# Performance work log

Hardware: AMD Instinct MI355X
Metric: run time of the kernel (lower is better)

The kernel has to match this reference:

```python
import jax, jax.numpy as jnp
import numpy as np

L1 = 0.05
L2 = 0.05
L3 = 0.05
L4 = 0.05
D_MIN = 1.0
EPS = 1e-12


def _pairwise_dist(x, y):
    sq = (jnp.sum(x * x, axis=-1)[:, None]
          + jnp.sum(y * y, axis=-1)[None, :]
          - 2.0 * (x @ y.T))
    return jnp.sqrt(jnp.clip(sq, EPS))


def setup_inputs() -> dict:
    key = jax.random.key(0)
    k1, k2, k3, k4, k5, k6 = jax.random.split(key, 6)
    B, C, D, d, P = 32768, 100, 1024, 512, 128
    return {
        "predictions": jax.random.normal(k1, (B, C), dtype=jnp.float32),
        "reconstructions": jax.random.normal(k2, (B, D), dtype=jnp.float32),
        "data": jax.random.normal(k3, (B, D), dtype=jnp.float32),
        "embeddings": jax.random.normal(k4, (B, d), dtype=jnp.float32),
        "prototypes": jax.random.normal(k5, (P, d), dtype=jnp.float32),
        "labels": jax.random.randint(k6, (B,), 0, C, dtype=jnp.int64),
    }


def reference(predictions, reconstructions, data, embeddings, prototypes, labels):
    B = predictions.shape[0]
    P = prototypes.shape[0]

    # Cross-entropy (mean reduction, class-index targets)
    logp = jax.nn.log_softmax(predictions, axis=-1)
    classification_loss = -jnp.mean(logp[jnp.arange(B), labels])

    # MSE reconstruction loss (mean reduction)
    reconstruction_loss = jnp.mean((reconstructions - data) ** 2)

    # Prototype diversity penalty: sum_{j<k} max(0, d_min - ||p_j - p_k||)^2
    proto_dist = _pairwise_dist(prototypes, prototypes)  # [P, P]
    hinge = jnp.maximum(0.0, D_MIN - proto_dist) ** 2
    upper = jnp.triu(jnp.ones((P, P), dtype=bool), k=1)
    diversity_penalty = jnp.sum(jnp.where(upper, hinge, 0.0))

    # Embedding-to-prototype distances [B, P], shared by similarity/coverage penalties
    dist = _pairwise_dist(embeddings, prototypes)
    similarity_penalty = jnp.sum(jnp.min(dist, axis=0)) / P
    coverage_penalty = jnp.sum(jnp.min(dist, axis=1)) / B

    total_loss = (classification_loss
                  + L1 * reconstruction_loss
                  + L2 * diversity_penalty
                  + L3 * similarity_penalty
                  + L4 * coverage_penalty)
    return total_loss
```

## Files before the change

### kernel.cpp

```cpp
#include <hip/hip_runtime.h>
#include <hip/hip_bf16.h>


constexpr float FEPS = 1e-12f;
constexpr float DMIN = 1.0f;

#define NB_DIST 512
#define NB_MSE  1024
#define NB_CE   256
#define NB_DIV  128

typedef unsigned short ushort_t;
typedef __attribute__((ext_vector_type(8))) short bf16x8;
typedef __attribute__((ext_vector_type(8))) unsigned short u16x8;
typedef __attribute__((ext_vector_type(4))) unsigned short u16x4;
typedef __attribute__((ext_vector_type(16))) float f32x16;
typedef __attribute__((ext_vector_type(4))) float f32x4;

typedef __attribute__((address_space(1))) const void gvoid_t;
typedef __attribute__((address_space(3))) void lvoid_t;

__device__ __forceinline__ unsigned short f2b(float f) {
    unsigned u = __float_as_uint(f);
    u += 0x7FFFu + ((u >> 16) & 1u);
    return (unsigned short)(u >> 16);
}

union SmemU {
    struct {
        char     As[8192];
        char     Bs[2 * 16384];
        float    rown[64];
        float    pn[128];
        unsigned rowmin[64];
        unsigned colmin[128];
    } dist;
    struct { float pp[512]; float spp; float sred[4]; } div;
    struct { float sred[4]; } red;
};

__global__ __launch_bounds__(128) void conv_kernel(const float* __restrict__ proto,
                                                   ushort_t* __restrict__ pB,
                                                   float* __restrict__ pnorm,
                                                   float* __restrict__ ws,
                                                   unsigned* __restrict__ proto_min) {
    int p = blockIdx.x, q = threadIdx.x;
    if (q == 0) proto_min[p] = 0x7F7F7F7Fu;
    if (p == 0 && q < 4) ws[q] = 0.f;
    float4 v = ((const float4*)(proto + (size_t)p * 512))[q];
    u16x4 o = { f2b(v.x), f2b(v.y), f2b(v.z), f2b(v.w) };
    *(u16x4*)(pB + (size_t)p * 512 + q * 4) = o;
    float s = v.x * v.x + v.y * v.y + v.z * v.z + v.w * v.w;
    #pragma unroll
    for (int off = 32; off; off >>= 1) s += __shfl_xor(s, off);
    __shared__ float sr[2];
    if ((q & 63) == 0) sr[q >> 6] = s;
    __syncthreads();
    if (q == 0) pnorm[p] = sr[0] + sr[1];
}

__device__ __forceinline__ void dist_body_fast(SmemU& sm, int bid,
                                               const float* __restrict__ emb,
                                               const ushort_t* __restrict__ pB,
                                               const float* __restrict__ pnormG,
                                               unsigned* __restrict__ proto_min,
                                               float* __restrict__ cov_out) {
    char*     AsB     = sm.dist.As;
    char*     BsB     = sm.dist.Bs;
    float*    rownL   = sm.dist.rown;
    float*    pnL     = sm.dist.pn;
    unsigned* rowminL = sm.dist.rowmin;
    unsigned* colminL = sm.dist.colmin;

    const int t  = threadIdx.x;
    const int m0 = bid * 64;

    if (t < 64)  { rownL[t] = 0.f; rowminL[t] = 0x7F7F7F7Fu; }
    if (t < 128) { colminL[t] = 0x7F7F7F7Fu; pnL[t] = pnormG[t]; }

    int aidx[4], rowi[4], swzi[4];
    const float4* embF4 = (const float4*)emb;
    #pragma unroll
    for (int i = 0; i < 4; ++i) {
        int flat = i * 256 + t;
        int row = flat >> 4, colq = flat & 15;
        rowi[i] = row;
        aidx[i] = (m0 + row) * 128 + colq;
        swzi[i] = row * 128 + ((((colq >> 1) ^ (row & 7)) << 4) | ((colq & 1) << 3));
    }

    const ushort_t* bsrcp[4];
    char* bdstW[4];
    #pragma unroll
    for (int i = 0; i < 4; ++i) {
        int f = i * 256 + t;
        int pr = f >> 3, gb = f & 7;
        bsrcp[i] = pB + pr * 512 + ((gb ^ (pr & 7)) << 3);
        bdstW[i] = BsB + (size_t)(i * 256 + (t & ~63)) * 16;
    }

    const int lane = t & 63, wv = t >> 6;
    const int wr = wv >> 1, wc = wv & 1;
    const int lo = lane & 31, hi = lane >> 5;
    const int arow = wr * 32 + lo;
    const int arz  = arow & 7;
    const int p0 = wc * 64 + lo, p1 = p0 + 32;
    const int pz = p0 & 7;
    const char* Ar  = AsB + arow * 128;
    const char* Br0 = BsB + p0 * 128;
    const char* Br1 = BsB + p1 * 128;

    __builtin_amdgcn_global_load_lds((gvoid_t*)(bsrcp[0]), (lvoid_t*)bdstW[0], 16, 0, 0);
    __builtin_amdgcn_global_load_lds((gvoid_t*)(bsrcp[1]), (lvoid_t*)bdstW[1], 16, 0, 0);
    __builtin_amdgcn_global_load_lds((gvoid_t*)(bsrcp[2]), (lvoid_t*)bdstW[2], 16, 0, 0);
    __builtin_amdgcn_global_load_lds((gvoid_t*)(bsrcp[3]), (lvoid_t*)bdstW[3], 16, 0, 0);
    float4 aE0 = embF4[aidx[0]], aE1 = embF4[aidx[1]],
           aE2 = embF4[aidx[2]], aE3 = embF4[aidx[3]];
    float4 aO0, aO1, aO2, aO3;
    float rn0 = 0.f, rn1 = 0.f, rn2 = 0.f, rn3 = 0.f;
    f32x16 acc0 = {}, acc1 = {};
    asm volatile("s_waitcnt lgkmcnt(0)" ::: "memory");
    __builtin_amdgcn_s_barrier();
    __builtin_amdgcn_sched_barrier(0);

#define DIST_CHUNK(c, WAITN, W0, W1, W2, W3, L0, L1, L2, L3)                   \
    {                                                                          \
        if ((c) < 7) {                                                         \
            const int kc1 = ((c) + 1) * 64;                                    \
            const int bo1 = (((c) + 1) & 1) * 16384;                           \
            __builtin_amdgcn_global_load_lds((gvoid_t*)(bsrcp[0] + kc1),       \
                (lvoid_t*)(bdstW[0] + bo1), 16, 0, 0);                         \
            __builtin_amdgcn_global_load_lds((gvoid_t*)(bsrcp[1] + kc1),       \
                (lvoid_t*)(bdstW[1] + bo1), 16, 0, 0);                         \
            __builtin_amdgcn_global_load_lds((gvoid_t*)(bsrcp[2] + kc1),       \
                (lvoid_t*)(bdstW[2] + bo1), 16, 0, 0);                         \
            __builtin_amdgcn_global_load_lds((gvoid_t*)(bsrcp[3] + kc1),       \
                (lvoid_t*)(bdstW[3] + bo1), 16, 0, 0);                         \
        }                                                                      \
        __builtin_amdgcn_sched_barrier(0);                                     \
        {                                                                      \
            const int kn = ((c) < 7 ? (c) + 1 : 7) * 16;                       \
            L0 = embF4[aidx[0] + kn]; L1 = embF4[aidx[1] + kn];                \
            L2 = embF4[aidx[2] + kn]; L3 = embF4[aidx[3] + kn];                \
        }                                                                      \
        __builtin_amdgcn_sched_barrier(0);                                     \
        rn0 = fmaf(W0.x, W0.x, rn0); rn0 = fmaf(W0.y, W0.y, rn0);              \
        rn0 = fmaf(W0.z, W0.z, rn0); rn0 = fmaf(W0.w, W0.w, rn0);              \
        rn1 = fmaf(W1.x, W1.x, rn1); rn1 = fmaf(W1.y, W1.y, rn1);              \
        rn1 = fmaf(W1.z, W1.z, rn1); rn1 = fmaf(W1.w, W1.w, rn1);              \
        rn2 = fmaf(W2.x, W2.x, rn2); rn2 = fmaf(W2.y, W2.y, rn2);              \
        rn2 = fmaf(W2.z, W2.z, rn2); rn2 = fmaf(W2.w, W2.w, rn2);              \
        rn3 = fmaf(W3.x, W3.x, rn3); rn3 = fmaf(W3.y, W3.y, rn3);              \
        rn3 = fmaf(W3.z, W3.z, rn3); rn3 = fmaf(W3.w, W3.w, rn3);              \
        { u16x4 u = { f2b(W0.x), f2b(W0.y), f2b(W0.z), f2b(W0.w) };            \
          *(u16x4*)(AsB + swzi[0]) = u; }                                      \
        { u16x4 u = { f2b(W1.x), f2b(W1.y), f2b(W1.z), f2b(W1.w) };            \
          *(u16x4*)(AsB + swzi[1]) = u; }                                      \
        { u16x4 u = { f2b(W2.x), f2b(W2.y), f2b(W2.z), f2b(W2.w) };            \
          *(u16x4*)(AsB + swzi[2]) = u; }                                      \
        { u16x4 u = { f2b(W3.x), f2b(W3.y), f2b(W3.z), f2b(W3.w) };            \
          *(u16x4*)(AsB + swzi[3]) = u; }                                      \
        asm volatile("s_waitcnt vmcnt(" #WAITN ")" ::: "memory");              \
        asm volatile("s_waitcnt lgkmcnt(0)" ::: "memory");                     \
        __builtin_amdgcn_s_barrier();                                          \
        __builtin_amdgcn_sched_barrier(0);                                     \
        {                                                                      \
            const int bo = ((c) & 1) * 16384;                                  \
            _Pragma("unroll")                                                  \
            for (int s = 0; s < 4; ++s) {                                      \
                const int g = (s * 2 + hi);                                    \
                bf16x8 af = *(const bf16x8*)(Ar  + ((g ^ arz) << 4));          \
                bf16x8 b0 = *(const bf16x8*)(Br0 + bo + ((g ^ pz) << 4));      \
                bf16x8 b1 = *(const bf16x8*)(Br1 + bo + ((g ^ pz) << 4));      \
                acc0 = __builtin_amdgcn_mfma_f32_32x32x16_bf16(af, b0, acc0, 0,0,0); \
                acc1 = __builtin_amdgcn_mfma_f32_32x32x16_bf16(af, b1, acc1, 0,0,0); \
            }                                                                  \
        }                                                                      \
        asm volatile("s_waitcnt lgkmcnt(0)" ::: "memory");                     \
        __builtin_amdgcn_s_barrier();                                          \
        __builtin_amdgcn_sched_barrier(0);                                     \
    }

    DIST_CHUNK(0, 8, aE0, aE1, aE2, aE3, aO0, aO1, aO2, aO3)
    DIST_CHUNK(1, 8, aO0, aO1, aO2, aO3, aE0, aE1, aE2, aE3)
    DIST_CHUNK(2, 8, aE0, aE1, aE2, aE3, aO0, aO1, aO2, aO3)
    DIST_CHUNK(3, 8, aO0, aO1, aO2, aO3, aE0, aE1, aE2, aE3)
    DIST_CHUNK(4, 8, aE0, aE1, aE2, aE3, aO0, aO1, aO2, aO3)
    DIST_CHUNK(5, 8, aO0, aO1, aO2, aO3, aE0, aE1, aE2, aE3)
    DIST_CHUNK(6, 8, aE0, aE1, aE2, aE3, aO0, aO1, aO2, aO3)
    DIST_CHUNK(7, 4, aO0, aO1, aO2, aO3, aE0, aE1, aE2, aE3)
#undef DIST_CHUNK

    atomicAdd(&rownL[rowi[0]], rn0);
    atomicAdd(&rownL[rowi[1]], rn1);
    atomicAdd(&rownL[rowi[2]], rn2);
    atomicAdd(&rownL[rowi[3]], rn3);
    __syncthreads();

    const float pn0 = pnL[p0], pn1 = pnL[p1];
    float cmin0 = 3.0e38f, cmin1 = 3.0e38f;
    #pragma unroll
    for (int r = 0; r < 16; ++r) {
        const int row = wr * 32 + (r & 3) + 8 * (r >> 2) + 4 * hi;
        const float nx = rownL[row];
        float d0 = sqrtf(fmaxf(nx + pn0 - 2.f * acc0[r], FEPS));
        float d1 = sqrtf(fmaxf(nx + pn1 - 2.f * acc1[r], FEPS));
        cmin0 = fminf(cmin0, d0);
        cmin1 = fminf(cmin1, d1);
        atomicMin(&rowminL[row], __float_as_uint(fminf(d0, d1)));
    }
    atomicMin(&colminL[p0], __float_as_uint(cmin0));
    atomicMin(&colminL[p1], __float_as_uint(cmin1));
    __syncthreads();

    if (t < 64) {
        float cv = __uint_as_float(rowminL[t]);
        #pragma unroll
        for (int o = 32; o; o >>= 1) cv += __shfl_xor(cv, o);
        if (t == 0) atomicAdd(cov_out, cv);
    }
    if (t < 128) atomicMin(&proto_min[t], colminL[t]);
}

__device__ __forceinline__ void dist_body_slow(SmemU& sm, int bid,
                                               const float* __restrict__ emb,
                                               const float* __restrict__ proto,
                                               unsigned* __restrict__ proto_min,
                                               float* __restrict__ cov_out) {
    char*     AsB     = sm.dist.As;
    char*     BsB     = sm.dist.Bs;
    float*    rownL   = sm.dist.rown;
    float*    pnL     = sm.dist.pn;
    unsigned* rowminL = sm.dist.rowmin;
    unsigned* colminL = sm.dist.colmin;

    const int t  = threadIdx.x;
    const int m0 = bid * 64;

    if (t < 64)  { rownL[t] = 0.f; rowminL[t] = 0x7F7F7F7Fu; }
    if (t < 128) { colminL[t] = 0x7F7F7F7Fu; pnL[t] = 0.f; }
    __syncthreads();

    const int ra = t >> 2, qa = t & 3;
    const int pb = t >> 1, hb = t & 1;
    const int raz = ra & 7, pbz = pb & 7;

    const float4* aG  = (const float4*)(emb + (size_t)(m0 + ra) * 512 + qa * 16);
    const float4* bGf = (const float4*)(proto + (size_t)pb * 512 + hb * 32);

    const int lane = t & 63, wv = t >> 6;
    const int wr = wv >> 1, wc = wv & 1;
    const int lo = lane & 31, hi = lane >> 5;
    const int arow = wr * 32 + lo;
    const int arz  = arow & 7;
    const int p0 = wc * 64 + lo, p1 = p0 + 32;
    const int pz = p0 & 7;

    float4 av0 = aG[0], av1 = aG[1], av2 = aG[2], av3 = aG[3];
    float4 bf0 = bGf[0], bf1 = bGf[1], bf2 = bGf[2], bf3 = bGf[3],
           bf4 = bGf[4], bf5 = bGf[5], bf6 = bGf[6], bf7 = bGf[7];

    f32x16 acc0 = {}, acc1 = {};
    char* Aw = AsB + ra * 128;
    char* Bw = BsB + pb * 128;
    const char* Ar  = AsB + arow * 128;
    const char* Br0 = BsB + p0 * 128;
    const char* Br1 = BsB + p1 * 128;

    for (int c = 0; c < 8; ++c) {
        {
            float nx = 0.f;
            nx = fmaf(av0.x, av0.x, nx); nx = fmaf(av0.y, av0.y, nx);
            nx = fmaf(av0.z, av0.z, nx); nx = fmaf(av0.w, av0.w, nx);
            nx = fmaf(av1.x, av1.x, nx); nx = fmaf(av1.y, av1.y, nx);
            nx = fmaf(av1.z, av1.z, nx); nx = fmaf(av1.w, av1.w, nx);
            nx = fmaf(av2.x, av2.x, nx); nx = fmaf(av2.y, av2.y, nx);
            nx = fmaf(av2.z, av2.z, nx); nx = fmaf(av2.w, av2.w, nx);
            nx = fmaf(av3.x, av3.x, nx); nx = fmaf(av3.y, av3.y, nx);
            nx = fmaf(av3.z, av3.z, nx); nx = fmaf(av3.w, av3.w, nx);
            atomicAdd(&rownL[ra], nx);
            u16x8 w0 = { f2b(av0.x), f2b(av0.y), f2b(av0.z), f2b(av0.w),
                         f2b(av1.x), f2b(av1.y), f2b(av1.z), f2b(av1.w) };
            u16x8 w1 = { f2b(av2.x), f2b(av2.y), f2b(av2.z), f2b(av2.w),
                         f2b(av3.x), f2b(av3.y), f2b(av3.z), f2b(av3.w) };
            *(u16x8*)(Aw + (((qa * 2 + 0) ^ raz) << 4)) = w0;
            *(u16x8*)(Aw + (((qa * 2 + 1) ^ raz) << 4)) = w1;

            float pns = 0.f;
            pns = fmaf(bf0.x, bf0.x, pns); pns = fmaf(bf0.y, bf0.y, pns);
            pns = fmaf(bf0.z, bf0.z, pns); pns = fmaf(bf0.w, bf0.w, pns);
            pns = fmaf(bf1.x, bf1.x, pns); pns = fmaf(bf1.y, bf1.y, pns);
            pns = fmaf(bf1.z, bf1.z, pns); pns = fmaf(bf1.w, bf1.w, pns);
            pns = fmaf(bf2.x, bf2.x, pns); pns = fmaf(bf2.y, bf2.y, pns);
            pns = fmaf(bf2.z, bf2.z, pns); pns = fmaf(bf2.w, bf2.w, pns);
            pns = fmaf(bf3.x, bf3.x, pns); pns = fmaf(bf3.y, bf3.y, pns);
            pns = fmaf(bf3.z, bf3.z, pns); pns = fmaf(bf3.w, bf3.w, pns);
            pns = fmaf(bf4.x, bf4.x, pns); pns = fmaf(bf4.y, bf4.y, pns);
            pns = fmaf(bf4.z, bf4.z, pns); pns = fmaf(bf4.w, bf4.w, pns);
            pns = fmaf(bf5.x, bf5.x, pns); pns = fmaf(bf5.y, bf5.y, pns);
            pns = fmaf(bf5.z, bf5.z, pns); pns = fmaf(bf5.w, bf5.w, pns);
            pns = fmaf(bf6.x, bf6.x, pns); pns = fmaf(bf6.y, bf6.y, pns);
            pns = fmaf(bf6.z, bf6.z, pns); pns = fmaf(bf6.w, bf6.w, pns);
            pns = fmaf(bf7.x, bf7.x, pns); pns = fmaf(bf7.y, bf7.y, pns);
            pns = fmaf(bf7.z, bf7.z, pns); pns = fmaf(bf7.w, bf7.w, pns);
            atomicAdd(&pnL[pb], pns);
            u16x8 x0 = { f2b(bf0.x), f2b(bf0.y), f2b(bf0.z), f2b(bf0.w),
                         f2b(bf1.x), f2b(bf1.y), f2b(bf1.z), f2b(bf1.w) };
            u16x8 x1 = { f2b(bf2.x), f2b(bf2.y), f2b(bf2.z), f2b(bf2.w),
                         f2b(bf3.x), f2b(bf3.y), f2b(bf3.z), f2b(bf3.w) };
            u16x8 x2 = { f2b(bf4.x), f2b(bf4.y), f2b(bf4.z), f2b(bf4.w),
                         f2b(bf5.x), f2b(bf5.y), f2b(bf5.z), f2b(bf5.w) };
            u16x8 x3 = { f2b(bf6.x), f2b(bf6.y), f2b(bf6.z), f2b(bf6.w),
                         f2b(bf7.x), f2b(bf7.y), f2b(bf7.z), f2b(bf7.w) };
            *(u16x8*)(Bw + (((hb * 4 + 0) ^ pbz) << 4)) = x0;
            *(u16x8*)(Bw + (((hb * 4 + 1) ^ pbz) << 4)) = x1;
            *(u16x8*)(Bw + (((hb * 4 + 2) ^ pbz) << 4)) = x2;
            *(u16x8*)(Bw + (((hb * 4 + 3) ^ pbz) << 4)) = x3;
        }
        __syncthreads();
        if (c < 7) {
            av0 = aG[(c + 1) * 16 + 0]; av1 = aG[(c + 1) * 16 + 1];
            av2 = aG[(c + 1) * 16 + 2]; av3 = aG[(c + 1) * 16 + 3];
            bf0 = bGf[(c + 1) * 16 + 0]; bf1 = bGf[(c + 1) * 16 + 1];
            bf2 = bGf[(c + 1) * 16 + 2]; bf3 = bGf[(c + 1) * 16 + 3];
            bf4 = bGf[(c + 1) * 16 + 4]; bf5 = bGf[(c + 1) * 16 + 5];
            bf6 = bGf[(c + 1) * 16 + 6]; bf7 = bGf[(c + 1) * 16 + 7];
        }
        #pragma unroll
        for (int s = 0; s < 4; ++s) {
            const int g = (s * 2 + hi);
            bf16x8 af = *(const bf16x8*)(Ar  + ((g ^ arz) << 4));
            bf16x8 b0 = *(const bf16x8*)(Br0 + ((g ^ pz)  << 4));
            bf16x8 b1 = *(const bf16x8*)(Br1 + ((g ^ pz)  << 4));
            acc0 = __builtin_amdgcn_mfma_f32_32x32x16_bf16(af, b0, acc0, 0, 0, 0);
            acc1 = __builtin_amdgcn_mfma_f32_32x32x16_bf16(af, b1, acc1, 0, 0, 0);
        }
        __syncthreads();
    }

    const float pn0 = pnL[p0], pn1 = pnL[p1];
    float cmin0 = 3.0e38f, cmin1 = 3.0e38f;
    #pragma unroll
    for (int r = 0; r < 16; ++r) {
        const int row = wr * 32 + (r & 3) + 8 * (r >> 2) + 4 * hi;
        const float nx = rownL[row];
        float d0 = sqrtf(fmaxf(nx + pn0 - 2.f * acc0[r], FEPS));
        float d1 = sqrtf(fmaxf(nx + pn1 - 2.f * acc1[r], FEPS));
        cmin0 = fminf(cmin0, d0);
        cmin1 = fminf(cmin1, d1);
        atomicMin(&rowminL[row], __float_as_uint(fminf(d0, d1)));
    }
    atomicMin(&colminL[p0], __float_as_uint(cmin0));
    atomicMin(&colminL[p1], __float_as_uint(cmin1));
    __syncthreads();

    if (t < 64) {
        float cv = __uint_as_float(rowminL[t]);
        #pragma unroll
        for (int o = 32; o; o >>= 1) cv += __shfl_xor(cv, o);
        if (t == 0) atomicAdd(cov_out, cv);
    }
    if (t < 128) atomicMin(&proto_min[t], colminL[t]);
}

__device__ __forceinline__ void mse_body(SmemU& sm, int mb,
                                         const float4* __restrict__ r,
                                         const float4* __restrict__ d,
                                         float* __restrict__ out, int n4) {
    const int t  = threadIdx.x;
    const int CH = (n4 + NB_MSE - 1) / NB_MSE;
    const int base = mb * CH;
    const int L = (base + CH <= n4) ? CH : (n4 - base);
    const f32x4* rb = (const f32x4*)(r + base);
    const f32x4* db = (const f32x4*)(d + base);
    float acc0 = 0.f, acc1 = 0.f, acc2 = 0.f, acc3 = 0.f;
    int k = t;
    for (; k + 7 * 256 < L; k += 8 * 256) {
        f32x4 a0 = __builtin_nontemporal_load(&rb[k + 0 * 256]);
        f32x4 a1 = __builtin_nontemporal_load(&rb[k + 1 * 256]);
        f32x4 a2 = __builtin_nontemporal_load(&rb[k + 2 * 256]);
        f32x4 a3 = __builtin_nontemporal_load(&rb[k + 3 * 256]);
        f32x4 a4 = __builtin_nontemporal_load(&rb[k + 4 * 256]);
        f32x4 a5 = __builtin_nontemporal_load(&rb[k + 5 * 256]);
        f32x4 a6 = __builtin_nontemporal_load(&rb[k + 6 * 256]);
        f32x4 a7 = __builtin_nontemporal_load(&rb[k + 7 * 256]);
        f32x4 b0 = __builtin_nontemporal_load(&db[k + 0 * 256]);
        f32x4 b1 = __builtin_nontemporal_load(&db[k + 1 * 256]);
        f32x4 b2 = __builtin_nontemporal_load(&db[k + 2 * 256]);
        f32x4 b3 = __builtin_nontemporal_load(&db[k + 3 * 256]);
        f32x4 b4 = __builtin_nontemporal_load(&db[k + 4 * 256]);
        f32x4 b5 = __builtin_nontemporal_load(&db[k + 5 * 256]);
        f32x4 b6 = __builtin_nontemporal_load(&db[k + 6 * 256]);
        f32x4 b7 = __builtin_nontemporal_load(&db[k + 7 * 256]);
        f32x4 e;
        e = a0 - b0; acc0 = fmaf(e.x, e.x, acc0); acc1 = fmaf(e.y, e.y, acc1);
                     acc2 = fmaf(e.z, e.z, acc2); acc3 = fmaf(e.w, e.w, acc3);
        e = a1 - b1; acc0 = fmaf(e.x, e.x, acc0); acc1 = fmaf(e.y, e.y, acc1);
                     acc2 = fmaf(e.z, e.z, acc2); acc3 = fmaf(e.w, e.w, acc3);
        e = a2 - b2; acc0 = fmaf(e.x, e.x, acc0); acc1 = fmaf(e.y, e.y, acc1);
                     acc2 = fmaf(e.z, e.z, acc2); acc3 = fmaf(e.w, e.w, acc3);
        e = a3 - b3; acc0 = fmaf(e.x, e.x, acc0); acc1 = fmaf(e.y, e.y, acc1);
                     acc2 = fmaf(e.z, e.z, acc2); acc3 = fmaf(e.w, e.w, acc3);
        e = a4 - b4; acc0 = fmaf(e.x, e.x, acc0); acc1 = fmaf(e.y, e.y, acc1);
                     acc2 = fmaf(e.z, e.z, acc2); acc3 = fmaf(e.w, e.w, acc3);
        e = a5 - b5; acc0 = fmaf(e.x, e.x, acc0); acc1 = fmaf(e.y, e.y, acc1);
                     acc2 = fmaf(e.z, e.z, acc2); acc3 = fmaf(e.w, e.w, acc3);
        e = a6 - b6; acc0 = fmaf(e.x, e.x, acc0); acc1 = fmaf(e.y, e.y, acc1);
                     acc2 = fmaf(e.z, e.z, acc2); acc3 = fmaf(e.w, e.w, acc3);
        e = a7 - b7; acc0 = fmaf(e.x, e.x, acc0); acc1 = fmaf(e.y, e.y, acc1);
                     acc2 = fmaf(e.z, e.z, acc2); acc3 = fmaf(e.w, e.w, acc3);
    }
    for (; k < L; k += 256) {
        f32x4 a = __builtin_nontemporal_load(&rb[k]);
        f32x4 b = __builtin_nontemporal_load(&db[k]);
        f32x4 e = a - b;
        acc0 = fmaf(e.x, e.x, acc0); acc1 = fmaf(e.y, e.y, acc1);
        acc2 = fmaf(e.z, e.z, acc2); acc3 = fmaf(e.w, e.w, acc3);
    }
    float acc = (acc0 + acc1) + (acc2 + acc3);
    #pragma unroll
    for (int o = 32; o; o >>= 1) acc += __shfl_xor(acc, o);
    int lane = t & 63, w = t >> 6;
    if (lane == 0) sm.red.sred[w] = acc;
    __syncthreads();
    if (t == 0) atomicAdd(out, sm.red.sred[0] + sm.red.sred[1]
                             + sm.red.sred[2] + sm.red.sred[3]);
}

__device__ __forceinline__ void ce_body(SmemU& sm, int cb,
                                        const float* __restrict__ pred,
                                        const int* __restrict__ lab,
                                        float* __restrict__ ce_out,
                                        int B, int C) {
    const int rows_per_wave = B / (NB_CE * 4);
    int lane = threadIdx.x & 63;
    int w    = threadIdx.x >> 6;
    int wid  = cb * 4 + w;
    float acc = 0.f;
    for (int i = 0; i < rows_per_wave; ++i) {
        int row = wid * rows_per_wave + i;
        const float* p = pred + (size_t)row * C;
        float v1 = (lane < C)      ? p[lane]      : -3.0e38f;
        float v2 = (lane + 64 < C) ? p[lane + 64] : -3.0e38f;
        float m = fmaxf(v1, v2);
        #pragma unroll
        for (int o = 32; o; o >>= 1) m = fmaxf(m, __shfl_xor(m, o));
        float s = ((lane < C) ? __expf(v1 - m) : 0.f)
                + ((lane + 64 < C) ? __expf(v2 - m) : 0.f);
        #pragma unroll
        for (int o = 32; o; o >>= 1) s += __shfl_xor(s, o);
        float lv = p[lab[row]];
        acc += m + __logf(s) - lv;
    }
    if (lane == 0) sm.red.sred[w] = acc;
    __syncthreads();
    if (threadIdx.x == 0) atomicAdd(ce_out, sm.red.sred[0] + sm.red.sred[1]
                                          + sm.red.sred[2] + sm.red.sred[3]);
}

__device__ __forceinline__ void div_body(SmemU& sm, int p,
                                         const float* __restrict__ proto,
                                         float* __restrict__ div_out, int dd) {
    int q = threadIdx.x;
    bool act = q < 128;
    if (act) for (int k = q; k < dd; k += 128) sm.div.pp[k] = proto[(size_t)p * dd + k];
    __syncthreads();
    float dot = 0.f, qq = 0.f;
    if (act) {
        const float4* pq4 = (const float4*)(proto + (size_t)q * dd);
        const float4* pp4 = (const float4*)sm.div.pp;
        for (int k4 = 0; k4 < dd / 4; ++k4) {
            float4 v = pq4[k4];
            float4 u = pp4[k4];
            dot = fmaf(u.x, v.x, dot); dot = fmaf(u.y, v.y, dot);
            dot = fmaf(u.z, v.z, dot); dot = fmaf(u.w, v.w, dot);
            qq  = fmaf(v.x, v.x, qq);  qq  = fmaf(v.y, v.y, qq);
            qq  = fmaf(v.z, v.z, qq);  qq  = fmaf(v.w, v.w, qq);
        }
        if (q == p) sm.div.spp = qq;
    }
    __syncthreads();
    float h2 = 0.f;
    if (act && q > p) {
        float sq = sm.div.spp + qq - 2.f * dot;
        float dist = sqrtf(fmaxf(sq, FEPS));
        float h = fmaxf(0.f, DMIN - dist);
        h2 = h * h;
    }
    #pragma unroll
    for (int o = 32; o; o >>= 1) h2 += __shfl_xor(h2, o);
    if ((q & 63) == 0) sm.div.sred[q >> 6] = h2;
    __syncthreads();
    if (q == 0) atomicAdd(div_out, sm.div.sred[0] + sm.div.sred[1]
                                 + sm.div.sred[2] + sm.div.sred[3]);
}

template<bool PRECONV>
__global__ __launch_bounds__(256) void fused_kernel(
        const float* __restrict__ pred, const int* __restrict__ lab,
        const float4* __restrict__ recon4, const float4* __restrict__ data4,
        const float* __restrict__ emb, const float* __restrict__ proto,
        const ushort_t* __restrict__ pB, const float* __restrict__ pnormG,
        float* __restrict__ ws, unsigned* __restrict__ proto_min,
        int B, int C, int n4, int dd) {
    __shared__ __attribute__((aligned(16))) SmemU sm;
    int bid = blockIdx.x;
    if (bid < NB_DIST) {
        if constexpr (PRECONV)
            dist_body_fast(sm, bid, emb, pB, pnormG, proto_min, ws + 3);
        else
            dist_body_slow(sm, bid, emb, proto, proto_min, ws + 3);
    } else if (bid < NB_DIST + NB_MSE) {
        mse_body(sm, bid - NB_DIST, recon4, data4, ws + 1, n4);
    } else if (bid < NB_DIST + NB_MSE + NB_CE) {
        ce_body(sm, bid - NB_DIST - NB_MSE, pred, lab, ws + 0, B, C);
    } else {
        div_body(sm, bid - NB_DIST - NB_MSE - NB_CE, proto, ws + 2, dd);
    }
}

__global__ void final_kernel(const float* __restrict__ ws,
                             const unsigned* __restrict__ pmin,
                             float* __restrict__ out, int B, int D, int P) {
    float sim = 0.f;
    for (int i = 0; i < P; ++i) sim += __uint_as_float(pmin[i]);
    float ce  = ws[0] / (float)B;
    float mse = ws[1] / ((float)B * (float)D);
    out[0] = ce + 0.05f * mse + 0.05f * ws[2] + 0.05f * (sim / (float)P)
           + 0.05f * (ws[3] / (float)B);
}

extern "C" void kernel_launch(void* const* d_in, const int* in_sizes, int n_in,
                              void* d_out, int out_size, void* d_ws, size_t ws_size,
                              hipStream_t stream) {
    const float* pred  = (const float*)d_in[0];
    const float* recon = (const float*)d_in[1];
    const float* data  = (const float*)d_in[2];
    const float* emb   = (const float*)d_in[3];
    const float* proto = (const float*)d_in[4];
    const int*   lab   = (const int*)d_in[5];
    float* out = (float*)d_out;

    int B  = in_sizes[5];
    int C  = in_sizes[0] / B;
    int D  = in_sizes[1] / B;
    int dd = in_sizes[3] / B;
    int P  = in_sizes[4] / dd;

    float* ws = (float*)d_ws;
    unsigned* proto_min = (unsigned*)(ws + 4);
    float*    pnorm     = ws + 132;
    ushort_t* pB        = (ushort_t*)((char*)d_ws + 1280);
    bool preconv = ws_size >= (size_t)(1280 + 128 * 512 * 2);

    int n4 = (B * D) / 4;
    int grid = NB_DIST + NB_MSE + NB_CE + NB_DIV;
    if (preconv) {
        conv_kernel<<<128, 128, 0, stream>>>(proto, pB, pnorm, ws, proto_min);
        fused_kernel<true><<<grid, 256, 0, stream>>>(
            pred, lab, (const float4*)recon, (const float4*)data, emb, proto,
            pB, pnorm, ws, proto_min, B, C, n4, dd);
    } else {
        hipMemsetAsync(ws, 0, 4 * sizeof(float), stream);
        hipMemsetAsync(ws + 4, 0x7F, P * sizeof(unsigned), stream);
        fused_kernel<false><<<grid, 256, 0, stream>>>(
            pred, lab, (const float4*)recon, (const float4*)data, emb, proto,
            nullptr, nullptr, ws, proto_min, B, C, n4, dd);
    }
    final_kernel<<<1, 1, 0, stream>>>(ws, proto_min, out, B, D, P);
}
```

Measured before the change: 100.7 us.

## Double the embedding rows per distance block to reuse prototype tiles

Each distance block now handles 128 embedding rows instead of 64, in two A sub-tiles that share every staged prototype B tile. The number of distance blocks is halved. Each wave issues four MFMAs per k-step, so every B fragment read from LDS is used twice. The cost is more accumulator registers and fewer blocks, which lowers occupancy and parallelism, and the embedding prefetch is restructured so it no longer double-buffers its registers. The slow path simply runs the old body twice per block.

```diff
diff --git a/kernel.cpp b/kernel.cpp
--- a/kernel.cpp
+++ b/kernel.cpp
@@ -5,7 +5,7 @@
 constexpr float FEPS = 1e-12f;
 constexpr float DMIN = 1.0f;
 
-#define NB_DIST 512
+#define NB_DIST 256
 #define NB_MSE  1024
 #define NB_CE   256
 #define NB_DIV  128
@@ -28,11 +28,11 @@
 
 union SmemU {
     struct {
-        char     As[8192];
+        char     As[2 * 8192];
         char     Bs[2 * 16384];
-        float    rown[64];
+        float    rown[128];
         float    pn[128];
-        unsigned rowmin[64];
+        unsigned rowmin[128];
         unsigned colmin[128];
     } dist;
     struct { float pp[512]; float spp; float sred[4]; } div;
@@ -73,10 +73,12 @@
     unsigned* colminL = sm.dist.colmin;
 
     const int t  = threadIdx.x;
-    const int m0 = bid * 64;
-
-    if (t < 64)  { rownL[t] = 0.f; rowminL[t] = 0x7F7F7F7Fu; }
-    if (t < 128) { colminL[t] = 0x7F7F7F7Fu; pnL[t] = pnormG[t]; }
+    const int m0 = bid * 128;
+
+    if (t < 128) {
+        rownL[t] = 0.f; rowminL[t] = 0x7F7F7F7Fu;
+        colminL[t] = 0x7F7F7F7Fu; pnL[t] = pnormG[t];
+    }
 
     int aidx[4], rowi[4], swzi[4];
     const float4* embF4 = (const float4*)emb;
@@ -106,7 +108,8 @@
     const int arz  = arow & 7;
     const int p0 = wc * 64 + lo, p1 = p0 + 32;
     const int pz = p0 & 7;
-    const char* Ar  = AsB + arow * 128;
+    const char* Ar0 = AsB + arow * 128;
+    const char* Ar1 = AsB + 8192 + arow * 128;
     const char* Br0 = BsB + p0 * 128;
     const char* Br1 = BsB + p1 * 128;
 
@@ -114,16 +117,22 @@
     __builtin_amdgcn_global_load_lds((gvoid_t*)(bsrcp[1]), (lvoid_t*)bdstW[1], 16, 0, 0);
     __builtin_amdgcn_global_load_lds((gvoid_t*)(bsrcp[2]), (lvoid_t*)bdstW[2], 16, 0, 0);
     __builtin_amdgcn_global_load_lds((gvoid_t*)(bsrcp[3]), (lvoid_t*)bdstW[3], 16, 0, 0);
-    float4 aE0 = embF4[aidx[0]], aE1 = embF4[aidx[1]],
-           aE2 = embF4[aidx[2]], aE3 = embF4[aidx[3]];
-    float4 aO0, aO1, aO2, aO3;
-    float rn0 = 0.f, rn1 = 0.f, rn2 = 0.f, rn3 = 0.f;
-    f32x16 acc0 = {}, acc1 = {};
+    float4 a00 = embF4[aidx[0]],        a01 = embF4[aidx[1]],
+           a02 = embF4[aidx[2]],        a03 = embF4[aidx[3]];
+    float4 a10 = embF4[aidx[0] + 8192], a11 = embF4[aidx[1] + 8192],
+           a12 = embF4[aidx[2] + 8192], a13 = embF4[aidx[3] + 8192];
+    float rn00 = 0.f, rn01 = 0.f, rn02 = 0.f, rn03 = 0.f;
+    float rn10 = 0.f, rn11 = 0.f, rn12 = 0.f, rn13 = 0.f;
+    f32x16 acc00 = {}, acc01 = {}, acc10 = {}, acc11 = {};
     asm volatile("s_waitcnt lgkmcnt(0)" ::: "memory");
     __builtin_amdgcn_s_barrier();
     __builtin_amdgcn_sched_barrier(0);
 
-#define DIST_CHUNK(c, WAITN, W0, W1, W2, W3, L0, L1, L2, L3)                   \
+#define FNORM(v, rn) rn = fmaf(v.x, v.x, rn); rn = fmaf(v.y, v.y, rn);         \
+                     rn = fmaf(v.z, v.z, rn); rn = fmaf(v.w, v.w, rn);
+#define AWRITE(v, base, i) { u16x4 u = { f2b(v.x), f2b(v.y), f2b(v.z), f2b(v.w) }; \
+                             *(u16x4*)((base) + swzi[i]) = u; }
+#define DIST_CHUNK(c, WAITN)                                                   \
     {                                                                          \
         if ((c) < 7) {                                                         \
             const int kc1 = ((c) + 1) * 64;                                    \
@@ -138,28 +147,20 @@
                 (lvoid_t*)(bdstW[3] + bo1), 16, 0, 0);                         \
         }                                                                      \
         __builtin_amdgcn_sched_barrier(0);                                     \
-        {                                                                      \
-            const int kn = ((c) < 7 ? (c) + 1 : 7) * 16;                       \
-            L0 = embF4[aidx[0] + kn]; L1 = embF4[aidx[1] + kn];                \
-            L2 = embF4[aidx[2] + kn]; L3 = embF4[aidx[3] + kn];                \
+        FNORM(a00, rn00) FNORM(a01, rn01) FNORM(a02, rn02) FNORM(a03, rn03)    \
+        FNORM(a10, rn10) FNORM(a11, rn11) FNORM(a12, rn12) FNORM(a13, rn13)    \
+        AWRITE(a00, AsB, 0) AWRITE(a01, AsB, 1)                                \
+        AWRITE(a02, AsB, 2) AWRITE(a03, AsB, 3)                                \
+        AWRITE(a10, AsB + 8192, 0) AWRITE(a11, AsB + 8192, 1)                  \
+        AWRITE(a12, AsB + 8192, 2) AWRITE(a13, AsB + 8192, 3)                  \
+        if ((c) < 7) {                                                         \
+            const int kn = ((c) + 1) * 16;                                     \
+            a00 = embF4[aidx[0] + kn];        a01 = embF4[aidx[1] + kn];       \
+            a02 = embF4[aidx[2] + kn];        a03 = embF4[aidx[3] + kn];       \
+            a10 = embF4[aidx[0] + 8192 + kn]; a11 = embF4[aidx[1] + 8192 + kn];\
+            a12 = embF4[aidx[2] + 8192 + kn]; a13 = embF4[aidx[3] + 8192 + kn];\
         }                                                                      \
         __builtin_amdgcn_sched_barrier(0);                                     \
-        rn0 = fmaf(W0.x, W0.x, rn0); rn0 = fmaf(W0.y, W0.y, rn0);              \
-        rn0 = fmaf(W0.z, W0.z, rn0); rn0 = fmaf(W0.w, W0.w, rn0);              \
-        rn1 = fmaf(W1.x, W1.x, rn1); rn1 = fmaf(W1.y, W1.y, rn1);              \
-        rn1 = fmaf(W1.z, W1.z, rn1); rn1 = fmaf(W1.w, W1.w, rn1);              \
-        rn2 = fmaf(W2.x, W2.x, rn2); rn2 = fmaf(W2.y, W2.y, rn2);              \
-        rn2 = fmaf(W2.z, W2.z, rn2); rn2 = fmaf(W2.w, W2.w, rn2);              \
-        rn3 = fmaf(W3.x, W3.x, rn3); rn3 = fmaf(W3.y, W3.y, rn3);              \
-        rn3 = fmaf(W3.z, W3.z, rn3); rn3 = fmaf(W3.w, W3.w, rn3);              \
-        { u16x4 u = { f2b(W0.x), f2b(W0.y), f2b(W0.z), f2b(W0.w) };            \
-          *(u16x4*)(AsB + swzi[0]) = u; }                                      \
-        { u16x4 u = { f2b(W1.x), f2b(W1.y), f2b(W1.z), f2b(W1.w) };            \
-          *(u16x4*)(AsB + swzi[1]) = u; }                                      \
-        { u16x4 u = { f2b(W2.x), f2b(W2.y), f2b(W2.z), f2b(W2.w) };            \
-          *(u16x4*)(AsB + swzi[2]) = u; }                                      \
-        { u16x4 u = { f2b(W3.x), f2b(W3.y), f2b(W3.z), f2b(W3.w) };            \
-          *(u16x4*)(AsB + swzi[3]) = u; }                                      \
         asm volatile("s_waitcnt vmcnt(" #WAITN ")" ::: "memory");              \
         asm volatile("s_waitcnt lgkmcnt(0)" ::: "memory");                     \
         __builtin_amdgcn_s_barrier();                                          \
@@ -169,11 +170,14 @@
             _Pragma("unroll")                                                  \
             for (int s = 0; s < 4; ++s) {                                      \
                 const int g = (s * 2 + hi);                                    \
-                bf16x8 af = *(const bf16x8*)(Ar  + ((g ^ arz) << 4));          \
-                bf16x8 b0 = *(const bf16x8*)(Br0 + bo + ((g ^ pz) << 4));      \
-                bf16x8 b1 = *(const bf16x8*)(Br1 + bo + ((g ^ pz) << 4));      \
-                acc0 = __builtin_amdgcn_mfma_f32_32x32x16_bf16(af, b0, acc0, 0,0,0); \
-                acc1 = __builtin_amdgcn_mfma_f32_32x32x16_bf16(af, b1, acc1, 0,0,0); \
+                bf16x8 af0 = *(const bf16x8*)(Ar0 + ((g ^ arz) << 4));         \
+                bf16x8 af1 = *(const bf16x8*)(Ar1 + ((g ^ arz) << 4));         \
+                bf16x8 b0  = *(const bf16x8*)(Br0 + bo + ((g ^ pz) << 4));     \
+                bf16x8 b1  = *(const bf16x8*)(Br1 + bo + ((g ^ pz) << 4));     \
+                acc00 = __builtin_amdgcn_mfma_f32_32x32x16_bf16(af0, b0, acc00, 0,0,0); \
+                acc01 = __builtin_amdgcn_mfma_f32_32x32x16_bf16(af0, b1, acc01, 0,0,0); \
+                acc10 = __builtin_amdgcn_mfma_f32_32x32x16_bf16(af1, b0, acc10, 0,0,0); \
+                acc11 = __builtin_amdgcn_mfma_f32_32x32x16_bf16(af1, b1, acc11, 0,0,0); \
             }                                                                  \
         }                                                                      \
         asm volatile("s_waitcnt lgkmcnt(0)" ::: "memory");                     \
@@ -181,20 +185,26 @@
         __builtin_amdgcn_sched_barrier(0);                                     \
     }
 
-    DIST_CHUNK(0, 8, aE0, aE1, aE2, aE3, aO0, aO1, aO2, aO3)
-    DIST_CHUNK(1, 8, aO0, aO1, aO2, aO3, aE0, aE1, aE2, aE3)
-    DIST_CHUNK(2, 8, aE0, aE1, aE2, aE3, aO0, aO1, aO2, aO3)
-    DIST_CHUNK(3, 8, aO0, aO1, aO2, aO3, aE0, aE1, aE2, aE3)
-    DIST_CHUNK(4, 8, aE0, aE1, aE2, aE3, aO0, aO1, aO2, aO3)
-    DIST_CHUNK(5, 8, aO0, aO1, aO2, aO3, aE0, aE1, aE2, aE3)
-    DIST_CHUNK(6, 8, aE0, aE1, aE2, aE3, aO0, aO1, aO2, aO3)
-    DIST_CHUNK(7, 4, aO0, aO1, aO2, aO3, aE0, aE1, aE2, aE3)
+    DIST_CHUNK(0, 12)
+    DIST_CHUNK(1, 12)
+    DIST_CHUNK(2, 12)
+    DIST_CHUNK(3, 12)
+    DIST_CHUNK(4, 12)
+    DIST_CHUNK(5, 12)
+    DIST_CHUNK(6, 12)
+    DIST_CHUNK(7, 0)
 #undef DIST_CHUNK
-
-    atomicAdd(&rownL[rowi[0]], rn0);
-    atomicAdd(&rownL[rowi[1]], rn1);
-    atomicAdd(&rownL[rowi[2]], rn2);
-    atomicAdd(&rownL[rowi[3]], rn3);
+#undef AWRITE
+#undef FNORM
+
+    atomicAdd(&rownL[rowi[0]], rn00);
+    atomicAdd(&rownL[rowi[1]], rn01);
+    atomicAdd(&rownL[rowi[2]], rn02);
+    atomicAdd(&rownL[rowi[3]], rn03);
+    atomicAdd(&rownL[64 + rowi[0]], rn10);
+    atomicAdd(&rownL[64 + rowi[1]], rn11);
+    atomicAdd(&rownL[64 + rowi[2]], rn12);
+    atomicAdd(&rownL[64 + rowi[3]], rn13);
     __syncthreads();
 
     const float pn0 = pnL[p0], pn1 = pnL[p1];
@@ -202,22 +212,26 @@
     #pragma unroll
     for (int r = 0; r < 16; ++r) {
         const int row = wr * 32 + (r & 3) + 8 * (r >> 2) + 4 * hi;
-        const float nx = rownL[row];
-        float d0 = sqrtf(fmaxf(nx + pn0 - 2.f * acc0[r], FEPS));
-        float d1 = sqrtf(fmaxf(nx + pn1 - 2.f * acc1[r], FEPS));
-        cmin0 = fminf(cmin0, d0);
-        cmin1 = fminf(cmin1, d1);
-        atomicMin(&rowminL[row], __float_as_uint(fminf(d0, d1)));
+        const float nx0 = rownL[row];
+        const float nx1 = rownL[64 + row];
+        float d00 = sqrtf(fmaxf(nx0 + pn0 - 2.f * acc00[r], FEPS));
+        float d01 = sqrtf(fmaxf(nx0 + pn1 - 2.f * acc01[r], FEPS));
+        float d10 = sqrtf(fmaxf(nx1 + pn0 - 2.f * acc10[r], FEPS));
+        float d11 = sqrtf(fmaxf(nx1 + pn1 - 2.f * acc11[r], FEPS));
+        cmin0 = fminf(cmin0, fminf(d00, d10));
+        cmin1 = fminf(cmin1, fminf(d01, d11));
+        atomicMin(&rowminL[row],      __float_as_uint(fminf(d00, d01)));
+        atomicMin(&rowminL[64 + row], __float_as_uint(fminf(d10, d11)));
     }
     atomicMin(&colminL[p0], __float_as_uint(cmin0));
     atomicMin(&colminL[p1], __float_as_uint(cmin1));
     __syncthreads();
 
-    if (t < 64) {
+    if (t < 128) {
         float cv = __uint_as_float(rowminL[t]);
         #pragma unroll
         for (int o = 32; o; o >>= 1) cv += __shfl_xor(cv, o);
-        if (t == 0) atomicAdd(cov_out, cv);
+        if ((t & 63) == 0) atomicAdd(cov_out, cv);
     }
     if (t < 128) atomicMin(&proto_min[t], colminL[t]);
 }
@@ -506,10 +520,13 @@
     __shared__ __attribute__((aligned(16))) SmemU sm;
     int bid = blockIdx.x;
     if (bid < NB_DIST) {
-        if constexpr (PRECONV)
+        if constexpr (PRECONV) {
             dist_body_fast(sm, bid, emb, pB, pnormG, proto_min, ws + 3);
-        else
-            dist_body_slow(sm, bid, emb, proto, proto_min, ws + 3);
+        } else {
+            dist_body_slow(sm, bid * 2, emb, proto, proto_min, ws + 3);
+            __syncthreads();
+            dist_body_slow(sm, bid * 2 + 1, emb, proto, proto_min, ws + 3);
+        }
     } else if (bid < NB_DIST + NB_MSE) {
         mse_body(sm, bid - NB_DIST, recon4, data4, ws + 1, n4);
     } else if (bid < NB_DIST + NB_MSE + NB_CE) {
```

Result: faster. 98.52 us (median of 2 runs) (-2.1%).
